# Performance work log

Hardware: AMD Instinct MI355X
Metric: run time of the kernel (lower is better)

Reference implementation:

```python
import jax, jax.numpy as jnp
import numpy as np

EMBED = 64
MAX_LEN = 256
EPS = 1e-5

def layernorm(x, g, b):
    mu = jnp.mean(x, axis=-1, keepdims=True)
    var = jnp.mean(jnp.square(x - mu), axis=-1, keepdims=True)
    return (x - mu) * jax.lax.rsqrt(var + EPS) * g + b

def setup_inputs() -> dict:
    key = jax.random.key(0)
    ks = jax.random.split(key, 10)
    V = 50257
    B, T = 32, 256
    s = 1.0 / np.sqrt(EMBED)
    return {
        "x": jax.random.randint(ks[0], (B, T), 0, V),
        "embed_w": jax.random.normal(ks[1], (V, EMBED), jnp.float32) * 0.02,
        "pos_w": jax.random.normal(ks[2], (MAX_LEN, EMBED), jnp.float32) * 0.02,
        "ln1_g": jnp.ones((EMBED,), jnp.float32),
        "ln1_b": jnp.zeros((EMBED,), jnp.float32),
        "Wq": jax.random.normal(ks[3], (EMBED, EMBED), jnp.float32) * s,
        "Wk": jax.random.normal(ks[4], (EMBED, EMBED), jnp.float32) * s,
        "Wv": jax.random.normal(ks[5], (EMBED, EMBED), jnp.float32) * s,
        "lnf_g": jnp.ones((EMBED,), jnp.float32),
        "lnf_b": jnp.zeros((EMBED,), jnp.float32),
        "fc_w": jax.random.normal(ks[6], (EMBED, V), jnp.float32) * s,
        "fc_b": jnp.zeros((V,), jnp.float32),
    }

def reference(x, embed_w, pos_w, ln1_g, ln1_b, Wq, Wk, Wv, lnf_g, lnf_b, fc_w, fc_b):
    B, T = x.shape
    tok = embed_w[x]                       # [B,T,E]
    pos = pos_w[:T][None, :, :]            # [1,T,E]
    h = tok + pos
    hn = layernorm(h, ln1_g, ln1_b)
    Q = hn @ Wq
    K = hn @ Wk
    V = hn @ Wv
    att = jnp.einsum('bqe,bke->bqk', Q, K) / jnp.sqrt(jnp.float32(EMBED))
    causal = jnp.tril(jnp.ones((T, T), bool))
    att = jnp.where(causal, att, -jnp.inf)
    att = jax.nn.softmax(att, axis=-1)
    ctx = jnp.einsum('bqk,bke->bqe', att, V)  # dropout = identity (eval mode)
    h = h + ctx
    h = layernorm(h, lnf_g, lnf_b)
    logits = h @ fc_w + fc_b               # [B,T,vocab]
    return logits
```

## Files before the change

kernel.cpp:

```cpp
#include <hip/hip_runtime.h>
#include <hip/hip_bf16.h>

#define EMBED  64
#define TLEN   256
#define BATCH  32
#define NROWS  (BATCH*TLEN)
#define VOCAB  50257
#define BCOLS  512
#define NB     99
#define VPAD   (NB*BCOLS)
#define LNEPS  1e-5f

typedef __attribute__((ext_vector_type(8))) short  bf16x8;
typedef __attribute__((ext_vector_type(4))) float  f32x4;
typedef __attribute__((ext_vector_type(4))) unsigned int u32x4;

static __device__ __forceinline__ unsigned short f2bf(float f) {
    unsigned int u = __float_as_uint(f);
    unsigned int r = (u + 0x7fffu + ((u >> 16) & 1u)) >> 16;
    return (unsigned short)r;
}

__global__ __launch_bounds__(256) void prep_wt(const float* __restrict__ fcw,
                                               unsigned short* __restrict__ wt) {
    int n = blockIdx.x * 256 + threadIdx.x;
    if (n >= VPAD) return;
    unsigned int packed[32];
    if (n < VOCAB) {
        #pragma unroll
        for (int k2 = 0; k2 < 32; ++k2) {
            unsigned int lo = f2bf(fcw[(size_t)(2*k2)   * VOCAB + n]);
            unsigned int hi = f2bf(fcw[(size_t)(2*k2+1) * VOCAB + n]);
            packed[k2] = lo | (hi << 16);
        }
    } else {
        #pragma unroll
        for (int k2 = 0; k2 < 32; ++k2) packed[k2] = 0u;
    }
    u32x4* dst = (u32x4*)(wt + (size_t)n * 64);
    #pragma unroll
    for (int i = 0; i < 8; ++i) {
        u32x4 v = { packed[4*i], packed[4*i+1], packed[4*i+2], packed[4*i+3] };
        dst[i] = v;
    }
}

__global__ __launch_bounds__(256) void embed_ln(const int* __restrict__ x,
                                                const float* __restrict__ ew,
                                                const float* __restrict__ pw,
                                                const float* __restrict__ g,
                                                const float* __restrict__ bb,
                                                float* __restrict__ h,
                                                float* __restrict__ hn) {
    int row = blockIdx.x * 4 + (threadIdx.x >> 6);
    int e   = threadIdx.x & 63;
    int tok = x[row];
    float v = ew[(size_t)tok * 64 + e] + pw[(size_t)(row & 255) * 64 + e];
    h[(size_t)row * 64 + e] = v;
    float s = v;
    #pragma unroll
    for (int m = 32; m >= 1; m >>= 1) s += __shfl_xor(s, m, 64);
    float mu = s * (1.f/64.f);
    float d  = v - mu;
    float s2 = d * d;
    #pragma unroll
    for (int m = 32; m >= 1; m >>= 1) s2 += __shfl_xor(s2, m, 64);
    float var = s2 * (1.f/64.f);
    hn[(size_t)row * 64 + e] = d * rsqrtf(var + LNEPS) * g[e] + bb[e];
}

__global__ __launch_bounds__(192) void qkv(const float* __restrict__ hn,
                                           const float* __restrict__ wq,
                                           const float* __restrict__ wk,
                                           const float* __restrict__ wv,
                                           float* __restrict__ q,
                                           float* __restrict__ kt,
                                           float* __restrict__ v) {
    int wave = threadIdx.x >> 6;
    int j    = threadIdx.x & 63;
    const float* W = (wave == 0) ? wq : ((wave == 1) ? wk : wv);
    int m0 = blockIdx.x * 16;
    for (int r = 0; r < 16; ++r) {
        int m = m0 + r;
        const float* hr = hn + (size_t)m * 64;
        float acc = 0.f;
        #pragma unroll
        for (int e = 0; e < 64; ++e) acc += hr[e] * W[e * 64 + j];
        if (wave == 0)      q[(size_t)m * 64 + j] = acc;
        else if (wave == 1) {
            int b = m >> 8, t = m & 255;
            kt[((size_t)b * 64 + j) * 256 + t] = acc;
        } else              v[(size_t)m * 64 + j] = acc;
    }
}

__global__ __launch_bounds__(256) void attn_sm(const float* __restrict__ q,
                                               const float* __restrict__ kt,
                                               float* __restrict__ p) {
    int b   = blockIdx.y;
    int m4  = blockIdx.x;
    int key = threadIdx.x;
    int wave = key >> 6, lane = key & 63;
    const float* ktb = kt + (size_t)b * 64 * 256;
    const float* qb  = q  + ((size_t)b * 256 + m4 * 4) * 64;
    float s0=0.f, s1=0.f, s2=0.f, s3=0.f;
    for (int e = 0; e < 64; ++e) {
        float kv = ktb[e * 256 + key];
        s0 += qb[e]       * kv;
        s1 += qb[64 + e]  * kv;
        s2 += qb[128 + e] * kv;
        s3 += qb[192 + e] * kv;
    }
    float sv[4] = { s0*0.125f, s1*0.125f, s2*0.125f, s3*0.125f };
    __shared__ float redm[4][4], reds[4][4];
    float pe[4];
    #pragma unroll
    for (int r = 0; r < 4; ++r) {
        int mrow = m4 * 4 + r;
        float xv = (key <= mrow) ? sv[r] : -1e30f;
        sv[r] = xv;
        float wm = xv;
        #pragma unroll
        for (int mm = 32; mm >= 1; mm >>= 1) wm = fmaxf(wm, __shfl_xor(wm, mm, 64));
        if (lane == 0) redm[wave][r] = wm;
    }
    __syncthreads();
    #pragma unroll
    for (int r = 0; r < 4; ++r) {
        float M = fmaxf(fmaxf(redm[0][r], redm[1][r]), fmaxf(redm[2][r], redm[3][r]));
        float e_ = expf(sv[r] - M);
        pe[r] = e_;
        float ws = e_;
        #pragma unroll
        for (int mm = 32; mm >= 1; mm >>= 1) ws += __shfl_xor(ws, mm, 64);
        if (lane == 0) reds[wave][r] = ws;
    }
    __syncthreads();
    float* pb = p + ((size_t)b * 256 + m4 * 4) * 256;
    #pragma unroll
    for (int r = 0; r < 4; ++r) {
        float S = reds[0][r] + reds[1][r] + reds[2][r] + reds[3][r];
        pb[r * 256 + key] = pe[r] / S;
    }
}

__global__ __launch_bounds__(256) void ctx_lnf(const float* __restrict__ p,
                                               const float* __restrict__ v,
                                               const float* __restrict__ h,
                                               const float* __restrict__ g,
                                               const float* __restrict__ bb,
                                               unsigned short* __restrict__ hf) {
    int m = blockIdx.x * 4 + (threadIdx.x >> 6);
    int n = threadIdx.x & 63;
    int b = m >> 8, t = m & 255;
    const float* pr = p + ((size_t)b * 256 + t) * 256;
    const float* vb = v + (size_t)b * 256 * 64;
    float acc = 0.f;
    for (int key = 0; key <= t; ++key)
        acc += pr[key] * vb[key * 64 + n];
    float h2 = h[(size_t)m * 64 + n] + acc;
    float s = h2;
    #pragma unroll
    for (int mm = 32; mm >= 1; mm >>= 1) s += __shfl_xor(s, mm, 64);
    float mu = s * (1.f/64.f);
    float d  = h2 - mu;
    float s2 = d * d;
    #pragma unroll
    for (int mm = 32; mm >= 1; mm >>= 1) s2 += __shfl_xor(s2, mm, 64);
    float var = s2 * (1.f/64.f);
    hf[(size_t)m * 64 + n] = f2bf(d * rsqrtf(var + LNEPS) * g[n] + bb[n]);
}

__global__ __launch_bounds__(256) void final_gemm(const unsigned short* __restrict__ hf,
                                                  const unsigned short* __restrict__ wt,
                                                  const float* __restrict__ bias,
                                                  float* __restrict__ out) {
    int bid = blockIdx.x;
    int xcd = bid & 7;
    int j   = bid >> 3;
    int g   = j / 792;
    int rj  = j - g * 792;
    int nb  = rj >> 3;
    int mb  = xcd * 64 + g * 8 + (rj & 7);

    int tid  = threadIdx.x;
    int wave = tid >> 6, lane = tid & 63;
    int l15 = lane & 15, lk = lane >> 4;
    int m0 = mb * 16;

    __shared__ float lds[16 * 520];

    const bf16x8* arow = (const bf16x8*)(hf + (size_t)(m0 + l15) * 64);
    bf16x8 a0 = arow[lk];
    bf16x8 a1 = arow[4 + lk];

    #pragma unroll
    for (int nt = 0; nt < 8; ++nt) {
        int lcol = wave * 128 + nt * 16 + l15;
        int col  = nb * BCOLS + lcol;
        const bf16x8* brow = (const bf16x8*)(wt + (size_t)col * 64);
        f32x4 c = {0.f, 0.f, 0.f, 0.f};
        c = __builtin_amdgcn_mfma_f32_16x16x32_bf16(a0, brow[lk],     c, 0, 0, 0);
        c = __builtin_amdgcn_mfma_f32_16x16x32_bf16(a1, brow[4 + lk], c, 0, 0, 0);
        float bv = (col < VOCAB) ? bias[col] : 0.f;
        #pragma unroll
        for (int r = 0; r < 4; ++r)
            lds[(lk * 4 + r) * 520 + lcol] = c[r] + bv;
    }
    __syncthreads();

    int row = tid >> 4, cc = tid & 15;
    float* orow = out + (size_t)(m0 + row) * VOCAB + nb * BCOLS;
    const float* lrow = lds + row * 520;
    #pragma unroll
    for (int i = 0; i < 8; ++i) {
        int lcol = i * 64 + cc * 4;
        f32x4 vv = *(const f32x4*)(lrow + lcol);
        int cs = nb * BCOLS + lcol;
        if (cs + 4 <= VOCAB) {
            *(f32x4*)(orow + lcol) = vv;
        } else {
            #pragma unroll
            for (int e = 0; e < 4; ++e)
                if (cs + e < VOCAB) orow[lcol + e] = vv[e];
        }
    }
}

extern "C" void kernel_launch(void* const* d_in, const int* in_sizes, int n_in,
                              void* d_out, int out_size, void* d_ws, size_t ws_size,
                              hipStream_t stream) {
    const int*   x    = (const int*)  d_in[0];
    const float* ew   = (const float*)d_in[1];
    const float* pw   = (const float*)d_in[2];
    const float* ln1g = (const float*)d_in[3];
    const float* ln1b = (const float*)d_in[4];
    const float* wq   = (const float*)d_in[5];
    const float* wk   = (const float*)d_in[6];
    const float* wv   = (const float*)d_in[7];
    const float* lnfg = (const float*)d_in[8];
    const float* lnfb = (const float*)d_in[9];
    const float* fcw  = (const float*)d_in[10];
    const float* fcb  = (const float*)d_in[11];
    float* out = (float*)d_out;

    char* ws = (char*)d_ws;
    float*          h  = (float*)(ws + 0);
    float*          hn = (float*)(ws + (2u<<20));
    unsigned short* hf = (unsigned short*)(ws + (2u<<20));
    float*          q  = (float*)(ws + (4u<<20));
    float*          kt = (float*)(ws + (6u<<20));
    float*          v  = (float*)(ws + (8u<<20));
    float*          p  = (float*)(ws + (10u<<20));
    unsigned short* wt = (unsigned short*)(ws + (18u<<20));

    prep_wt  <<<dim3(VPAD / 256),  dim3(256), 0, stream>>>(fcw, wt);
    embed_ln <<<dim3(NROWS / 4),   dim3(256), 0, stream>>>(x, ew, pw, ln1g, ln1b, h, hn);
    qkv      <<<dim3(NROWS / 16),  dim3(192), 0, stream>>>(hn, wq, wk, wv, q, kt, v);
    attn_sm  <<<dim3(64, 32),      dim3(256), 0, stream>>>(q, kt, p);
    ctx_lnf  <<<dim3(NROWS / 4),   dim3(256), 0, stream>>>(p, v, h, lnfg, lnfb, hf);
    final_gemm<<<dim3(8 * 8 * NB * 8), dim3(256), 0, stream>>>(hf, wt, fcb, out);
}
```

Baseline: 643.8 us.

## Make final GEMM persistent with double-buffered LDS staging over column strips

```diff
diff --git a/kernel.cpp b/kernel.cpp
--- a/kernel.cpp
+++ b/kernel.cpp
@@ -6,9 +6,9 @@
 #define BATCH  32
 #define NROWS  (BATCH*TLEN)
 #define VOCAB  50257
-#define BCOLS  512
-#define NB     99
-#define VPAD   (NB*BCOLS)
+#define SCOLS  256
+#define NSTR   198
+#define VPAD   (NSTR*SCOLS)
 #define LNEPS  1e-5f
 
 typedef __attribute__((ext_vector_type(8))) short  bf16x8;
@@ -175,55 +175,77 @@
                                                   const unsigned short* __restrict__ wt,
                                                   const float* __restrict__ bias,
                                                   float* __restrict__ out) {
-    int bid = blockIdx.x;
-    int xcd = bid & 7;
-    int j   = bid >> 3;
-    int g   = j / 792;
-    int rj  = j - g * 792;
-    int nb  = rj >> 3;
-    int mb  = xcd * 64 + g * 8 + (rj & 7);
+    int bid  = blockIdx.x;
+    int xcd  = bid & 7;
+    int t_   = bid >> 3;
+    int half = t_ & 1;
+    int sl   = t_ >> 1;
+    int mb   = xcd * 64 + sl;
+    int m0   = mb * 16;
+    int s0   = half * (NSTR / 2);
+    int sN   = NSTR / 2;
 
     int tid  = threadIdx.x;
     int wave = tid >> 6, lane = tid & 63;
     int l15 = lane & 15, lk = lane >> 4;
-    int m0 = mb * 16;
-
-    __shared__ float lds[16 * 520];
+
+    __shared__ float lds[2][16][260];
 
     const bf16x8* arow = (const bf16x8*)(hf + (size_t)(m0 + l15) * 64);
     bf16x8 a0 = arow[lk];
     bf16x8 a1 = arow[4 + lk];
 
-    #pragma unroll
-    for (int nt = 0; nt < 8; ++nt) {
-        int lcol = wave * 128 + nt * 16 + l15;
-        int col  = nb * BCOLS + lcol;
+    int srow = tid >> 4, scc = tid & 15;
+    float* orow = out + (size_t)(m0 + srow) * VOCAB;
+
+    #pragma unroll
+    for (int nt = 0; nt < 4; ++nt) {
+        int lcol = wave * 64 + nt * 16 + l15;
+        int col  = s0 * SCOLS + lcol;
         const bf16x8* brow = (const bf16x8*)(wt + (size_t)col * 64);
         f32x4 c = {0.f, 0.f, 0.f, 0.f};
         c = __builtin_amdgcn_mfma_f32_16x16x32_bf16(a0, brow[lk],     c, 0, 0, 0);
         c = __builtin_amdgcn_mfma_f32_16x16x32_bf16(a1, brow[4 + lk], c, 0, 0, 0);
         float bv = (col < VOCAB) ? bias[col] : 0.f;
         #pragma unroll
-        for (int r = 0; r < 4; ++r)
-            lds[(lk * 4 + r) * 520 + lcol] = c[r] + bv;
-    }
-    __syncthreads();
-
-    int row = tid >> 4, cc = tid & 15;
-    float* orow = out + (size_t)(m0 + row) * VOCAB + nb * BCOLS;
-    const float* lrow = lds + row * 520;
-    #pragma unroll
-    for (int i = 0; i < 8; ++i) {
-        int lcol = i * 64 + cc * 4;
-        f32x4 vv = *(const f32x4*)(lrow + lcol);
-        int cs = nb * BCOLS + lcol;
-        if (cs + 4 <= VOCAB) {
-            *(f32x4*)(orow + lcol) = vv;
-        } else {
+        for (int r = 0; r < 4; ++r) lds[0][lk * 4 + r][lcol] = c[r] + bv;
+    }
+
+    int cur = 0;
+    for (int s = 0; s < sN; ++s) {
+        __syncthreads();
+        if (s + 1 < sN) {
             #pragma unroll
-            for (int e = 0; e < 4; ++e)
-                if (cs + e < VOCAB) orow[lcol + e] = vv[e];
+            for (int nt = 0; nt < 4; ++nt) {
+                int lcol = wave * 64 + nt * 16 + l15;
+                int col  = (s0 + s + 1) * SCOLS + lcol;
+                const bf16x8* brow = (const bf16x8*)(wt + (size_t)col * 64);
+                f32x4 c = {0.f, 0.f, 0.f, 0.f};
+                c = __builtin_amdgcn_mfma_f32_16x16x32_bf16(a0, brow[lk],     c, 0, 0, 0);
+                c = __builtin_amdgcn_mfma_f32_16x16x32_bf16(a1, brow[4 + lk], c, 0, 0, 0);
+                float bv = (col < VOCAB) ? bias[col] : 0.f;
+                #pragma unroll
+                for (int r = 0; r < 4; ++r) lds[cur ^ 1][lk * 4 + r][lcol] = c[r] + bv;
+            }
         }
+        {
+            int cbase = (s0 + s) * SCOLS;
+            const float* lrow = &lds[cur][srow][0];
+            #pragma unroll
+            for (int i = 0; i < 4; ++i) {
+                int lcol = i * 64 + scc * 4;
+                f32x4 vv = *(const f32x4*)(lrow + lcol);
+                int cs = cbase + lcol;
+                if (cs + 4 <= VOCAB) {
+                    *(f32x4*)(orow + cs) = vv;
+                } else {
+                    #pragma unroll
+                    for (int e = 0; e < 4; ++e)
+                        if (cs + e < VOCAB) orow[cs + e] = vv[e];
+                }
+            }
+        }
+        cur ^= 1;
     }
 }
 
@@ -259,5 +281,5 @@
     qkv      <<<dim3(NROWS / 16),  dim3(192), 0, stream>>>(hn, wq, wk, wv, q, kt, v);
     attn_sm  <<<dim3(64, 32),      dim3(256), 0, stream>>>(q, kt, p);
     ctx_lnf  <<<dim3(NROWS / 4),   dim3(256), 0, stream>>>(p, v, h, lnfg, lnfb, hf);
-    final_gemm<<<dim3(8 * 8 * NB * 8), dim3(256), 0, stream>>>(hf, wt, fcb, out);
-}
+    final_gemm<<<dim3(1024),       dim3(256), 0, stream>>>(hf, wt, fcb, out);
+}
```

After: 871.2 us. 1.35x slower.

## Make final GEMM persistent per row block with double-buffered LDS stripes

Applied to the files above, without the earlier changes.

```diff
diff --git a/kernel.cpp b/kernel.cpp
--- a/kernel.cpp
+++ b/kernel.cpp
@@ -6,9 +6,9 @@
 #define BATCH  32
 #define NROWS  (BATCH*TLEN)
 #define VOCAB  50257
-#define BCOLS  512
-#define NB     99
-#define VPAD   (NB*BCOLS)
+#define SCOLS  512
+#define NSTR   99
+#define VPAD   (NSTR*SCOLS)
 #define LNEPS  1e-5f
 
 typedef __attribute__((ext_vector_type(8))) short  bf16x8;
@@ -171,59 +171,78 @@
     hf[(size_t)m * 64 + n] = f2bf(d * rsqrtf(var + LNEPS) * g[n] + bb[n]);
 }
 
-__global__ __launch_bounds__(256) void final_gemm(const unsigned short* __restrict__ hf,
-                                                  const unsigned short* __restrict__ wt,
-                                                  const float* __restrict__ bias,
-                                                  float* __restrict__ out) {
+__global__ __launch_bounds__(256, 2) void final_gemm(const unsigned short* __restrict__ hf,
+                                                     const unsigned short* __restrict__ wt,
+                                                     const float* __restrict__ bias,
+                                                     float* __restrict__ out) {
     int bid = blockIdx.x;
     int xcd = bid & 7;
-    int j   = bid >> 3;
-    int g   = j / 792;
-    int rj  = j - g * 792;
-    int nb  = rj >> 3;
-    int mb  = xcd * 64 + g * 8 + (rj & 7);
+    int mb  = xcd * 64 + (bid >> 3);
+    int m0  = mb * 16;
 
     int tid  = threadIdx.x;
     int wave = tid >> 6, lane = tid & 63;
     int l15 = lane & 15, lk = lane >> 4;
-    int m0 = mb * 16;
-
-    __shared__ float lds[16 * 520];
-
-    const bf16x8* arow = (const bf16x8*)(hf + (size_t)(m0 + l15) * 64);
-    bf16x8 a0 = arow[lk];
-    bf16x8 a1 = arow[4 + lk];
-
-    #pragma unroll
-    for (int nt = 0; nt < 8; ++nt) {
-        int lcol = wave * 128 + nt * 16 + l15;
-        int col  = nb * BCOLS + lcol;
-        const bf16x8* brow = (const bf16x8*)(wt + (size_t)col * 64);
-        f32x4 c = {0.f, 0.f, 0.f, 0.f};
-        c = __builtin_amdgcn_mfma_f32_16x16x32_bf16(a0, brow[lk],     c, 0, 0, 0);
-        c = __builtin_amdgcn_mfma_f32_16x16x32_bf16(a1, brow[4 + lk], c, 0, 0, 0);
-        float bv = (col < VOCAB) ? bias[col] : 0.f;
-        #pragma unroll
-        for (int r = 0; r < 4; ++r)
-            lds[(lk * 4 + r) * 520 + lcol] = c[r] + bv;
-    }
-    __syncthreads();
-
-    int row = tid >> 4, cc = tid & 15;
-    float* orow = out + (size_t)(m0 + row) * VOCAB + nb * BCOLS;
-    const float* lrow = lds + row * 520;
-    #pragma unroll
-    for (int i = 0; i < 8; ++i) {
-        int lcol = i * 64 + cc * 4;
-        f32x4 vv = *(const f32x4*)(lrow + lcol);
-        int cs = nb * BCOLS + lcol;
-        if (cs + 4 <= VOCAB) {
-            *(f32x4*)(orow + lcol) = vv;
-        } else {
-            #pragma unroll
-            for (int e = 0; e < 4; ++e)
-                if (cs + e < VOCAB) orow[lcol + e] = vv[e];
+
+    __shared__ float lds[2][16][520];
+
+    const bf16x8* hrow = (const bf16x8*)(hf + (size_t)(m0 + l15) * 64);
+    bf16x8 hb0 = hrow[lk];
+    bf16x8 hb1 = hrow[4 + lk];
+
+    int srow = tid >> 4, scc = tid & 15;
+    float* orow = out + (size_t)(m0 + srow) * VOCAB;
+
+    auto computeS = [&](int s, int buf) {
+        int cbase = s * SCOLS;
+        #pragma unroll
+        for (int nt = 0; nt < 8; ++nt) {
+            int lcol = wave * 128 + nt * 16;
+            int wr   = cbase + lcol + l15;
+            const bf16x8* wrow = (const bf16x8*)(wt + (size_t)wr * 64);
+            f32x4 c = {0.f, 0.f, 0.f, 0.f};
+            c = __builtin_amdgcn_mfma_f32_16x16x32_bf16(wrow[lk],     hb0, c, 0, 0, 0);
+            c = __builtin_amdgcn_mfma_f32_16x16x32_bf16(wrow[4 + lk], hb1, c, 0, 0, 0);
+            int bc = cbase + lcol + lk * 4;
+            if (bc + 4 <= VOCAB) {
+                f32x4 bv = *(const f32x4*)(bias + bc);
+                c += bv;
+            } else {
+                #pragma unroll
+                for (int e = 0; e < 4; ++e)
+                    c[e] += (bc + e < VOCAB) ? bias[bc + e] : 0.f;
+            }
+            *(f32x4*)&lds[buf][l15][lcol + lk * 4] = c;
         }
+    };
+
+    auto storeS = [&](int s, int buf) {
+        int cbase = s * SCOLS;
+        const float* lrow = &lds[buf][srow][0];
+        #pragma unroll
+        for (int i = 0; i < 8; ++i) {
+            int lcol = i * 64 + scc * 4;
+            f32x4 vv = *(const f32x4*)(lrow + lcol);
+            int cs = cbase + lcol;
+            if (cs + 4 <= VOCAB) {
+                *(f32x4*)(orow + cs) = vv;
+            } else {
+                #pragma unroll
+                for (int e = 0; e < 4; ++e)
+                    if (cs + e < VOCAB) orow[cs + e] = vv[e];
+            }
+        }
+    };
+
+    computeS(0, 0);
+    int cur = 0;
+    for (int s = 0; s < NSTR; ++s) {
+        asm volatile("s_waitcnt lgkmcnt(0)" ::: "memory");
+        __builtin_amdgcn_s_barrier();
+        __builtin_amdgcn_sched_barrier(0);
+        if (s + 1 < NSTR) computeS(s + 1, cur ^ 1);
+        storeS(s, cur);
+        cur ^= 1;
     }
 }
 
@@ -259,5 +278,5 @@
     qkv      <<<dim3(NROWS / 16),  dim3(192), 0, stream>>>(hn, wq, wk, wv, q, kt, v);
     attn_sm  <<<dim3(64, 32),      dim3(256), 0, stream>>>(q, kt, p);
     ctx_lnf  <<<dim3(NROWS / 4),   dim3(256), 0, stream>>>(p, v, h, lnfg, lnfb, hf);
-    final_gemm<<<dim3(8 * 8 * NB * 8), dim3(256), 0, stream>>>(hf, wt, fcb, out);
-}
+    final_gemm<<<dim3(512),        dim3(256), 0, stream>>>(hf, wt, fcb, out);
+}
```

Measured after the change: 1.116 ms. +73.3%, slower.

## Halve final GEMM column tile and swap MFMA operands for vectorized LDS writes

Applied to the files above, without the earlier changes.

```diff
diff --git a/kernel.cpp b/kernel.cpp
--- a/kernel.cpp
+++ b/kernel.cpp
@@ -6,8 +6,8 @@
 #define BATCH  32
 #define NROWS  (BATCH*TLEN)
 #define VOCAB  50257
-#define BCOLS  512
-#define NB     99
+#define BCOLS  256
+#define NB     198
 #define VPAD   (NB*BCOLS)
 #define LNEPS  1e-5f
 
@@ -178,45 +178,50 @@
     int bid = blockIdx.x;
     int xcd = bid & 7;
     int j   = bid >> 3;
-    int g   = j / 792;
-    int rj  = j - g * 792;
+    int g   = j / 1584;
+    int rj  = j - g * 1584;
     int nb  = rj >> 3;
     int mb  = xcd * 64 + g * 8 + (rj & 7);
+    int m0  = mb * 16;
+    int cb  = nb * BCOLS;
 
     int tid  = threadIdx.x;
     int wave = tid >> 6, lane = tid & 63;
     int l15 = lane & 15, lk = lane >> 4;
-    int m0 = mb * 16;
-
-    __shared__ float lds[16 * 520];
-
-    const bf16x8* arow = (const bf16x8*)(hf + (size_t)(m0 + l15) * 64);
-    bf16x8 a0 = arow[lk];
-    bf16x8 a1 = arow[4 + lk];
-
-    #pragma unroll
-    for (int nt = 0; nt < 8; ++nt) {
-        int lcol = wave * 128 + nt * 16 + l15;
-        int col  = nb * BCOLS + lcol;
-        const bf16x8* brow = (const bf16x8*)(wt + (size_t)col * 64);
+
+    __shared__ float lds[16][260];
+
+    const bf16x8* hrow = (const bf16x8*)(hf + (size_t)(m0 + l15) * 64);
+    bf16x8 hb0 = hrow[lk];
+    bf16x8 hb1 = hrow[4 + lk];
+
+    #pragma unroll
+    for (int nt = 0; nt < 4; ++nt) {
+        int lcol = wave * 64 + nt * 16;
+        const bf16x8* wrow = (const bf16x8*)(wt + (size_t)(cb + lcol + l15) * 64);
         f32x4 c = {0.f, 0.f, 0.f, 0.f};
-        c = __builtin_amdgcn_mfma_f32_16x16x32_bf16(a0, brow[lk],     c, 0, 0, 0);
-        c = __builtin_amdgcn_mfma_f32_16x16x32_bf16(a1, brow[4 + lk], c, 0, 0, 0);
-        float bv = (col < VOCAB) ? bias[col] : 0.f;
-        #pragma unroll
-        for (int r = 0; r < 4; ++r)
-            lds[(lk * 4 + r) * 520 + lcol] = c[r] + bv;
+        c = __builtin_amdgcn_mfma_f32_16x16x32_bf16(wrow[lk],     hb0, c, 0, 0, 0);
+        c = __builtin_amdgcn_mfma_f32_16x16x32_bf16(wrow[4 + lk], hb1, c, 0, 0, 0);
+        int bc = cb + lcol + lk * 4;
+        if (bc + 4 <= VOCAB) {
+            c += *(const f32x4*)(bias + bc);
+        } else {
+            #pragma unroll
+            for (int e = 0; e < 4; ++e)
+                c[e] += (bc + e < VOCAB) ? bias[bc + e] : 0.f;
+        }
+        *(f32x4*)&lds[l15][lcol + lk * 4] = c;
     }
     __syncthreads();
 
     int row = tid >> 4, cc = tid & 15;
-    float* orow = out + (size_t)(m0 + row) * VOCAB + nb * BCOLS;
-    const float* lrow = lds + row * 520;
-    #pragma unroll
-    for (int i = 0; i < 8; ++i) {
+    float* orow = out + (size_t)(m0 + row) * VOCAB + cb;
+    const float* lrow = &lds[row][0];
+    #pragma unroll
+    for (int i = 0; i < 4; ++i) {
         int lcol = i * 64 + cc * 4;
         f32x4 vv = *(const f32x4*)(lrow + lcol);
-        int cs = nb * BCOLS + lcol;
+        int cs = cb + lcol;
         if (cs + 4 <= VOCAB) {
             *(f32x4*)(orow + lcol) = vv;
         } else {
```

Result: slower. 695.4 us (+8.0%).
